# Kernel optimization log

Hardware: AMD Instinct MI355X
Metric: run time of the kernel (lower is better)

Reference implementation:

```python
import jax, jax.numpy as jnp
import numpy as np

VOCAB = 50000
DIM = 300
PAD_ID = 0
UNK_ID = 1
CTX_W = 2  # context_window
B, S = 32, 4096


def setup_inputs() -> dict:
    key = jax.random.key(0)
    k_ids, k_unk, k_tab = jax.random.split(key, 3)
    input_ids = jax.random.randint(k_ids, (B, S), 0, VOCAB, dtype=jnp.int64)
    unk_mask = jax.random.uniform(k_unk, (B, S)) < 0.05
    input_ids = jnp.where(unk_mask, UNK_ID, input_ids)
    table = jax.random.normal(k_tab, (VOCAB, DIM), dtype=jnp.float32)
    # pad row is zero, as in the torch constructor
    table = table.at[PAD_ID].set(0.0)
    return {"input_ids": input_ids, "table": table}


def reference(input_ids, table):
    # embedding gather: [B, S, D]
    emb = table[input_ids]
    dtype = table.dtype
    seq_len = input_ids.shape[1]
    win = 2 * CTX_W + 1

    # valid = not UNK and not PAD (same mask used inside every window)
    valid = ((input_ids != UNK_ID) & (input_ids != PAD_ID)).astype(dtype)  # [B, S]
    masked_emb = emb * valid[..., None]

    # zero-pad seq dim by CTX_W on both sides (torch pads embeddings with 0
    # and ids with pad_id, which is masked out -> equivalent to zero pad)
    pe = jnp.pad(masked_emb, ((0, 0), (CTX_W, CTX_W), (0, 0)))
    pm = jnp.pad(valid, ((0, 0), (CTX_W, CTX_W)))

    # sliding-window masked sum/count over window of size 2w+1 (includes
    # center, which is UNK at replaced positions and thus masked anyway).
    # Context uses ORIGINAL gathered embeddings (torch builds padded copy
    # before its in-place loop), so a plain windowed sum is faithful.
    wsum = sum(pe[:, k:k + seq_len] for k in range(win))   # [B, S, D]
    wcnt = sum(pm[:, k:k + seq_len] for k in range(win))   # [B, S]

    avg_ctx = wsum / (wcnt[..., None] + 1e-8)
    is_unk = (input_ids == UNK_ID)[..., None]
    return jnp.where(is_unk, avg_ctx, emb)
```

## Files before the change

kernel.cpp:

```cpp
#include <hip/hip_runtime.h>


#define PAD_ID 0
#define UNK_ID 1
#define SEQ    4096
#define DIM4   75
#define ITEMS  4

typedef float vf4 __attribute__((ext_vector_type(4)));

__global__ __launch_bounds__(256) void w2v_embed_kernel(
    const int* __restrict__ ids,
    const vf4* __restrict__ table4,
    vf4* __restrict__ out4,
    int total4)
{
    const int tid  = threadIdx.x;
    const int base = blockIdx.x * (256 * ITEMS) + tid;

    int   ii[ITEMS], tt[ITEMS], dd[ITEMS], idv[ITEMS];
    bool  ok[ITEMS];

#pragma unroll
    for (int u = 0; u < ITEMS; ++u) {
        int i = base + u * 256;
        ii[u] = i;
        ok[u] = (i < total4);
        int t = i / DIM4;
        tt[u] = t;
        dd[u] = i - t * DIM4;
        idv[u] = ok[u] ? ids[t] : 0;
    }

    vf4 val[ITEMS];
#pragma unroll
    for (int u = 0; u < ITEMS; ++u) {
        val[u] = ok[u] ? table4[idv[u] * DIM4 + dd[u]] : (vf4)0.f;
    }

#pragma unroll
    for (int u = 0; u < ITEMS; ++u) {
        if (ok[u] && idv[u] == UNK_ID) {
            int t = tt[u], d = dd[u];
            int s = t & (SEQ - 1);
            vf4 acc = (vf4)0.f;
            float cnt = 0.f;
#pragma unroll
            for (int k = -2; k <= 2; ++k) {
                if (k == 0) continue;
                int sn = s + k;
                if (sn < 0 || sn >= SEQ) continue;
                int idn = ids[t + k];
                if (idn == PAD_ID || idn == UNK_ID) continue;
                acc += table4[idn * DIM4 + d];
                cnt += 1.f;
            }
            float inv = 1.f / (cnt + 1e-8f);
            val[u] = acc * inv;
        }
    }

#pragma unroll
    for (int u = 0; u < ITEMS; ++u) {
        if (ok[u]) __builtin_nontemporal_store(val[u], &out4[ii[u]]);
    }
}

extern "C" void kernel_launch(void* const* d_in, const int* in_sizes, int n_in,
                              void* d_out, int out_size, void* d_ws, size_t ws_size,
                              hipStream_t stream)
{
    const int* ids    = (const int*)d_in[0];
    const vf4* table4 = (const vf4*)d_in[1];
    vf4*       out4   = (vf4*)d_out;

    int total4 = out_size / 4;
    int per_block = 256 * ITEMS;
    int grid = (total4 + per_block - 1) / per_block;
    w2v_embed_kernel<<<grid, 256, 0, stream>>>(ids, table4, out4, total4);
}
```

Baseline: 216.7 us.

## Template guard-free kernel, raise items per thread, and branchless UNK neighbor gathers

Makes the kernel a template over items-per-thread and a bounds-guard flag. When the total divides evenly it launches a guard-free version with 8 items per thread instead of 4. Non-UNK results are stored right away, and UNK positions are recomputed afterwards. That path loads the neighbour ids first, folds PAD/UNK/out-of-range neighbours into the zero PAD row so all four row loads are issued unconditionally, then counts the valid ones. The aim is more memory loads in flight per thread and less divergent branching, at the cost of higher register pressure.

```diff
diff --git a/kernel.cpp b/kernel.cpp
--- a/kernel.cpp
+++ b/kernel.cpp
@@ -5,64 +5,75 @@
 #define UNK_ID 1
 #define SEQ    4096
 #define DIM4   75
-#define ITEMS  4
+#define TPB    256
 
 typedef float vf4 __attribute__((ext_vector_type(4)));
 
-__global__ __launch_bounds__(256) void w2v_embed_kernel(
+template <int ITEMS, bool GUARD>
+__global__ __launch_bounds__(TPB) void w2v_embed_kernel(
     const int* __restrict__ ids,
     const vf4* __restrict__ table4,
     vf4* __restrict__ out4,
     int total4)
 {
     const int tid  = threadIdx.x;
-    const int base = blockIdx.x * (256 * ITEMS) + tid;
+    const int base = blockIdx.x * (TPB * ITEMS) + tid;
 
-    int   ii[ITEMS], tt[ITEMS], dd[ITEMS], idv[ITEMS];
-    bool  ok[ITEMS];
+    int ii[ITEMS], tt[ITEMS], dd[ITEMS], idv[ITEMS];
 
 #pragma unroll
     for (int u = 0; u < ITEMS; ++u) {
-        int i = base + u * 256;
+        int i = base + u * TPB;
         ii[u] = i;
-        ok[u] = (i < total4);
-        int t = i / DIM4;
+        int t = (int)((unsigned)i / DIM4);
         tt[u] = t;
         dd[u] = i - t * DIM4;
-        idv[u] = ok[u] ? ids[t] : 0;
+        idv[u] = (!GUARD || i < total4) ? ids[t] : PAD_ID;
     }
 
     vf4 val[ITEMS];
 #pragma unroll
     for (int u = 0; u < ITEMS; ++u) {
-        val[u] = ok[u] ? table4[idv[u] * DIM4 + dd[u]] : (vf4)0.f;
+        val[u] = table4[idv[u] * DIM4 + dd[u]];
     }
 
 #pragma unroll
     for (int u = 0; u < ITEMS; ++u) {
-        if (ok[u] && idv[u] == UNK_ID) {
-            int t = tt[u], d = dd[u];
-            int s = t & (SEQ - 1);
-            vf4 acc = (vf4)0.f;
-            float cnt = 0.f;
-#pragma unroll
-            for (int k = -2; k <= 2; ++k) {
-                if (k == 0) continue;
-                int sn = s + k;
-                if (sn < 0 || sn >= SEQ) continue;
-                int idn = ids[t + k];
-                if (idn == PAD_ID || idn == UNK_ID) continue;
-                acc += table4[idn * DIM4 + d];
-                cnt += 1.f;
-            }
-            float inv = 1.f / (cnt + 1e-8f);
-            val[u] = acc * inv;
-        }
+        if ((!GUARD || ii[u] < total4) && idv[u] != UNK_ID)
+            __builtin_nontemporal_store(val[u], &out4[ii[u]]);
     }
 
 #pragma unroll
     for (int u = 0; u < ITEMS; ++u) {
-        if (ok[u]) __builtin_nontemporal_store(val[u], &out4[ii[u]]);
+        if (idv[u] == UNK_ID) {
+            const int t = tt[u], d = dd[u];
+            const int s = t & (SEQ - 1);
+
+            int idn[4];
+            const int off0[4] = {-2, -1, 1, 2};
+#pragma unroll
+            for (int j = 0; j < 4; ++j) {
+                int sn = s + off0[j];
+                bool in = (sn >= 0) && (sn < SEQ);
+                int x = ids[in ? (t + off0[j]) : t];
+                idn[j] = (in && x != UNK_ID) ? x : PAD_ID;
+            }
+
+            vf4 row[4];
+#pragma unroll
+            for (int j = 0; j < 4; ++j)
+                row[j] = table4[idn[j] * DIM4 + d];
+
+            float cnt = 0.f;
+            vf4 acc = (vf4)0.f;
+#pragma unroll
+            for (int j = 0; j < 4; ++j) {
+                acc += row[j];
+                cnt += (idn[j] != PAD_ID) ? 1.f : 0.f;
+            }
+            vf4 r = acc * (1.f / (cnt + 1e-8f));
+            __builtin_nontemporal_store(r, &out4[ii[u]]);
+        }
     }
 }
 
@@ -75,7 +86,15 @@
     vf4*       out4   = (vf4*)d_out;
 
     int total4 = out_size / 4;
-    int per_block = 256 * ITEMS;
-    int grid = (total4 + per_block - 1) / per_block;
-    w2v_embed_kernel<<<grid, 256, 0, stream>>>(ids, table4, out4, total4);
+    constexpr int ITEMS = 8;
+    const int per_block = TPB * ITEMS;
+
+    if (total4 % per_block == 0) {
+        w2v_embed_kernel<ITEMS, false>
+            <<<total4 / per_block, TPB, 0, stream>>>(ids, table4, out4, total4);
+    } else {
+        int grid = (total4 + per_block - 1) / per_block;
+        w2v_embed_kernel<ITEMS, true>
+            <<<grid, TPB, 0, stream>>>(ids, table4, out4, total4);
+    }
 }
```

After: 218.3 us. Within noise of the previous version (+0.8%).
